# Kernel tuning notes

Hardware: AMD Instinct MI355X
Metric: run time of the kernel (lower is better)

## Reference

```python
import jax, jax.numpy as jnp
import numpy as np

IGNORE_INDEX = -100


def setup_inputs() -> dict:
    key = jax.random.key(0)
    k1, k2, k3 = jax.random.split(key, 3)
    BT, H, V = 2048, 2048, 128000
    x = jax.random.normal(k1, (BT, H), dtype=jnp.float32)
    weight = jax.random.normal(k2, (V, H), dtype=jnp.float32) * (1.0 / np.sqrt(H))
    target = jax.random.randint(k3, (BT,), 0, V, dtype=jnp.int64)
    return {"x": x, "weight": weight, "target": target}


def reference(x, weight, target):
    # Fused linear + cross-entropy forward (reduction='mean').
    # logits: [BT, V], accumulated in fp32 like the helion kernel.
    logits = jnp.einsum("bh,vh->bv", x.astype(jnp.float32), weight.astype(jnp.float32))
    lse = jax.nn.logsumexp(logits, axis=-1)  # [BT]
    target_logit = jnp.take_along_axis(logits, target[:, None], axis=-1)[:, 0]
    valid = (target != IGNORE_INDEX)
    nll = (lse - target_logit) * valid.astype(jnp.float32)  # [BT]
    n_non_ignore = valid.sum().astype(jnp.float32)
    loss = nll.sum() / n_non_ignore
    return loss.astype(x.dtype), lse
```

## Files before the change

### kernel.cpp

```cpp
#include <hip/hip_runtime.h>
#include <hip/hip_bf16.h>


typedef __bf16 bf16x8 __attribute__((ext_vector_type(8)));
typedef float f32x4  __attribute__((ext_vector_type(4)));
typedef float f32x16 __attribute__((ext_vector_type(16)));

#define BM 128
#define BN 128
#define BK 32
#define LDK 40

__device__ __forceinline__ unsigned pkbf(float a, float b) {
  __hip_bfloat162 h = __float22bfloat162_rn(float2{a, b});
  unsigned r;
  __builtin_memcpy(&r, &h, 4);
  return r;
}

__device__ __forceinline__ void gl16(const void* g, const void* l) {
  using GP = const unsigned __attribute__((address_space(1)))*;
  using LP = unsigned __attribute__((address_space(3)))*;
  __builtin_amdgcn_global_load_lds((GP)(unsigned long long)g,
                                   (LP)(unsigned)(unsigned long long)l, 16, 0, 0);
}

__global__ __launch_bounds__(256)
void k_cvt256(const float* __restrict__ src, __bf16* __restrict__ dst, int H, int NT)
{
  const int bid = blockIdx.x;
  const int kt = bid % NT;
  const int r = threadIdx.x;
  const float* s = src + (size_t)((bid / NT) * 256 + r) * H + kt * 64;
  __bf16* d = dst + (size_t)bid * 16384;
  #pragma unroll
  for (int j = 0; j < 8; ++j) {
    float4 f0 = ((const float4*)s)[2 * j];
    float4 f1 = ((const float4*)s)[2 * j + 1];
    uint4 p;
    p.x = pkbf(f0.x, f0.y); p.y = pkbf(f0.z, f0.w);
    p.z = pkbf(f1.x, f1.y); p.w = pkbf(f1.z, f1.w);
    *(uint4*)(d + (j >> 2) * 8192 + (j & 3) * 2048 + r * 8) = p;
  }
}

__global__ __launch_bounds__(256)
void k_tgt(const float* __restrict__ x, const float* __restrict__ w,
           const int* __restrict__ tgt, float* __restrict__ ws_t, int H)
{
  const int row  = blockIdx.x * 4 + (threadIdx.x >> 6);
  const int lane = threadIdx.x & 63;
  const int tv = tgt[row];
  if (tv == -100) { if (lane == 0) ws_t[row] = 0.f; return; }
  const float* xr = x + (size_t)row * H;
  const float* wr = w + (size_t)tv * H;
  float acc = 0.f;
  for (int j = lane * 4; j < H; j += 256) {
    float4 a = *(const float4*)(xr + j);
    float4 b = *(const float4*)(wr + j);
    acc += a.x * b.x + a.y * b.y + a.z * b.z + a.w * b.w;
  }
  #pragma unroll
  for (int m = 1; m < 64; m <<= 1) acc += __shfl_xor(acc, m, 64);
  if (lane == 0) ws_t[row] = acc;
}

#define VM8 asm volatile("s_waitcnt vmcnt(8)" ::: "memory");
#define VM4 asm volatile("s_waitcnt vmcnt(4)" ::: "memory");
#define VM0 asm volatile("s_waitcnt vmcnt(0)" ::: "memory");
#define NOVM
#define MEMFENCE asm volatile("" ::: "memory");

#define SLOT(SL, SLN, BCUR, BNXT, DO_ST, ST_S, DO_RA, VMW)                      \
  {                                                                             \
    __builtin_amdgcn_s_barrier();                                               \
    MEMFENCE                                                                    \
    if (DO_ST) stage_slot(ST_S);                                                \
    _Pragma("unroll")                                                           \
    for (int m = 0; m < 4; ++m)                                                 \
      a1[m] = *(const bf16x8*)&As[SL][kcoff + (arow + (m + 4) * 16) * 8];       \
    __builtin_amdgcn_s_setprio(1);                                              \
    _Pragma("unroll")                                                           \
    for (int m = 0; m < 4; ++m)                                                 \
      _Pragma("unroll")                                                         \
      for (int n = 0; n < 4; ++n)                                               \
        acc[m][n] = __builtin_amdgcn_mfma_f32_16x16x32_bf16(a0[m], BCUR[n],     \
                                                            acc[m][n], 0, 0, 0);\
    __builtin_amdgcn_s_setprio(0);                                              \
    VMW                                                                         \
    __builtin_amdgcn_s_barrier();                                               \
    MEMFENCE                                                                    \
    if (DO_RA) {                                                                \
      _Pragma("unroll")                                                         \
      for (int m = 0; m < 4; ++m)                                               \
        a0[m] = *(const bf16x8*)&As[SLN][kcoff + (arow + m * 16) * 8];          \
      _Pragma("unroll")                                                         \
      for (int n = 0; n < 4; ++n)                                               \
        BNXT[n] = *(const bf16x8*)&Bs[SLN][kcoff + (bcol + n * 16) * 8];        \
    }                                                                           \
    __builtin_amdgcn_s_setprio(1);                                              \
    _Pragma("unroll")                                                           \
    for (int m = 0; m < 4; ++m)                                                 \
      _Pragma("unroll")                                                         \
      for (int n = 0; n < 4; ++n)                                               \
        acc[m + 4][n] = __builtin_amdgcn_mfma_f32_16x16x32_bf16(a1[m], BCUR[n], \
                                                         acc[m + 4][n], 0, 0, 0);\
    __builtin_amdgcn_s_setprio(0);                                              \
  }

__global__ __launch_bounds__(512, 2)
void k_gemm16(const __bf16* __restrict__ xb, const __bf16* __restrict__ wb,
              float* __restrict__ ws_m, float* __restrict__ ws_s,
              int NT, int NCB, int ROWB)
{
  __shared__ __bf16 As[4][8192];
  __shared__ __bf16 Bs[4][8192];

  int wg = blockIdx.x;
  const int nwg = gridDim.x;
  if ((nwg & 7) == 0) wg = (wg & 7) * (nwg >> 3) + (wg >> 3);
  const int rowb = wg % ROWB;
  const int cb   = wg / ROWB;
  const int row0 = rowb * 256;

  const int t    = threadIdx.x;
  const int lane = t & 63;
  const int wv   = t >> 6;
  const int wr   = wv >> 2;
  const int wc   = wv & 3;

  const int kcoff = (lane >> 4) * 2048;
  const int arow  = wr * 128 + (lane & 15);
  const int bcol  = wc * 64 + (lane & 15);

  const __bf16* ga = xb + (size_t)(rowb * NT) * 16384;
  const __bf16* gb = wb + (size_t)(cb * NT) * 16384;

  auto stage_slot = [&](int s) {
    const int ph = s & 3;
    const size_t off = (size_t)(s >> 1) * 16384 + (size_t)(s & 1) * 8192
                     + wv * 512 + lane * 8;
    const __bf16* a = ga + off;
    const __bf16* b = gb + off;
    gl16(a,        &As[ph][wv * 512]);
    gl16(a + 4096, &As[ph][4096 + wv * 512]);
    gl16(b,        &Bs[ph][wv * 512]);
    gl16(b + 4096, &Bs[ph][4096 + wv * 512]);
  };

  const int S = NT * 2;

  stage_slot(0); stage_slot(1); stage_slot(2);
  VM8
  __builtin_amdgcn_s_barrier();
  MEMFENCE

  f32x4 acc[8][4] = {};
  bf16x8 a0[4], a1[4], b0[4], b1[4];
  #pragma unroll
  for (int m = 0; m < 4; ++m)
    a0[m] = *(const bf16x8*)&As[0][kcoff + (arow + m * 16) * 8];
  #pragma unroll
  for (int n = 0; n < 4; ++n)
    b0[n] = *(const bf16x8*)&Bs[0][kcoff + (bcol + n * 16) * 8];

  for (int g = 0; g < (S - 4) / 4; ++g) {
    const int j0 = g * 4;
    SLOT(0, 1, b0, b1, true, j0 + 3, true, VM8)
    SLOT(1, 2, b1, b0, true, j0 + 4, true, VM8)
    SLOT(2, 3, b0, b1, true, j0 + 5, true, VM8)
    SLOT(3, 0, b1, b0, true, j0 + 6, true, VM8)
  }
  SLOT(0, 1, b0, b1, true,  S - 1, true,  VM8)
  SLOT(1, 2, b1, b0, false, 0,     true,  VM4)
  SLOT(2, 3, b0, b1, false, 0,     true,  VM0)
  SLOT(3, 0, b1, b0, false, 0,     false, NOVM)

  __syncthreads();

  float* redM = (float*)&As[0][0];
  float* redS = redM + 1024;
  const int g4 = (lane >> 4) * 4;
  #pragma unroll
  for (int m = 0; m < 8; ++m) {
    #pragma unroll
    for (int r = 0; r < 4; ++r) {
      const int rl = wr * 128 + m * 16 + g4 + r;
      float mx = fmaxf(fmaxf(acc[m][0][r], acc[m][1][r]),
                       fmaxf(acc[m][2][r], acc[m][3][r]));
      #pragma unroll
      for (int sh = 1; sh < 16; sh <<= 1) mx = fmaxf(mx, __shfl_xor(mx, sh, 64));
      float sv = 0.f;
      #pragma unroll
      for (int n = 0; n < 4; ++n) sv += expf(acc[m][n][r] - mx);
      #pragma unroll
      for (int sh = 1; sh < 16; sh <<= 1) sv += __shfl_xor(sv, sh, 64);
      if ((lane & 15) == 0) { redM[wc * 256 + rl] = mx; redS[wc * 256 + rl] = sv; }
    }
  }
  __syncthreads();
  if (t < 256) {
    const float m0 = redM[t], m1 = redM[256 + t], m2 = redM[512 + t], m3 = redM[768 + t];
    float M = fmaxf(fmaxf(m0, m1), fmaxf(m2, m3));
    float S2 = redS[t] * expf(m0 - M) + redS[256 + t] * expf(m1 - M)
             + redS[512 + t] * expf(m2 - M) + redS[768 + t] * expf(m3 - M);
    const int grow = row0 + t;
    ws_m[(size_t)grow * NCB + cb] = M;
    ws_s[(size_t)grow * NCB + cb] = S2;
  }
}

__global__ __launch_bounds__(256, 2)
void k_gemm_lse(const float* __restrict__ x, const float* __restrict__ w,
                const int* __restrict__ tgt,
                float* __restrict__ ws_m, float* __restrict__ ws_s,
                float* __restrict__ ws_t,
                int H, int NCB, int ROWB)
{
  __shared__ unsigned short As[2][BM * LDK];
  __shared__ unsigned short Bs[2][BN * LDK];

  const int bid  = blockIdx.x;
  const int rowb = bid % ROWB;
  const int cb   = bid / ROWB;
  const int row0 = rowb * BM;
  const int col0 = cb * BN;

  const int t    = threadIdx.x;
  const int lane = t & 63;
  const int wv   = t >> 6;
  const int sr = t >> 1;
  const int sk = (t & 1) * 16;

  const float* xa = x + (size_t)(row0 + sr) * H + sk;
  const float* wb = w + (size_t)(col0 + sr) * H + sk;

  float4 ra[4], rb[4];
  #pragma unroll
  for (int i = 0; i < 4; ++i) {
    ra[i] = *(const float4*)(xa + i * 4);
    rb[i] = *(const float4*)(wb + i * 4);
  }

  auto stage = [&](int buf) {
    uint4 p0, p1;
    p0.x = pkbf(ra[0].x, ra[0].y); p0.y = pkbf(ra[0].z, ra[0].w);
    p0.z = pkbf(ra[1].x, ra[1].y); p0.w = pkbf(ra[1].z, ra[1].w);
    p1.x = pkbf(ra[2].x, ra[2].y); p1.y = pkbf(ra[2].z, ra[2].w);
    p1.z = pkbf(ra[3].x, ra[3].y); p1.w = pkbf(ra[3].z, ra[3].w);
    *(uint4*)&As[buf][sr * LDK + sk]     = p0;
    *(uint4*)&As[buf][sr * LDK + sk + 8] = p1;
    p0.x = pkbf(rb[0].x, rb[0].y); p0.y = pkbf(rb[0].z, rb[0].w);
    p0.z = pkbf(rb[1].x, rb[1].y); p0.w = pkbf(rb[1].z, rb[1].w);
    p1.x = pkbf(rb[2].x, rb[2].y); p1.y = pkbf(rb[2].z, rb[2].w);
    p1.z = pkbf(rb[3].x, rb[3].y); p1.w = pkbf(rb[3].z, rb[3].w);
    *(uint4*)&Bs[buf][sr * LDK + sk]     = p0;
    *(uint4*)&Bs[buf][sr * LDK + sk + 8] = p1;
  };

  stage(0);
  __syncthreads();

  f32x16 acc[4] = {};
  const int rlo = lane & 31;
  const int hi  = lane >> 5;
  const int NT  = H / BK;
  int cur = 0;

  for (int kt = 0; kt < NT; ++kt) {
    const bool pf = (kt + 1 < NT);
    if (pf) {
      xa += BK; wb += BK;
      #pragma unroll
      for (int i = 0; i < 4; ++i) {
        ra[i] = *(const float4*)(xa + i * 4);
        rb[i] = *(const float4*)(wb + i * 4);
      }
    }
    const unsigned short* A = As[cur];
    const unsigned short* B = Bs[cur];
    #pragma unroll
    for (int ks = 0; ks < 2; ++ks) {
      const int koff = ks * 16 + hi * 8;
      bf16x8 a = *(const bf16x8*)&A[(wv * 32 + rlo) * LDK + koff];
      #pragma unroll
      for (int nf = 0; nf < 4; ++nf) {
        bf16x8 b = *(const bf16x8*)&B[(nf * 32 + rlo) * LDK + koff];
        acc[nf] = __builtin_amdgcn_mfma_f32_32x32x16_bf16(a, b, acc[nf], 0, 0, 0);
      }
    }
    if (pf) stage(cur ^ 1);
    __syncthreads();
    cur ^= 1;
  }

  #pragma unroll
  for (int reg = 0; reg < 16; ++reg) {
    const int row = wv * 32 + (reg & 3) + 8 * (reg >> 2) + 4 * hi;
    float mx = fmaxf(fmaxf(acc[0][reg], acc[1][reg]), fmaxf(acc[2][reg], acc[3][reg]));
    #pragma unroll
    for (int m = 1; m < 32; m <<= 1) mx = fmaxf(mx, __shfl_xor(mx, m, 64));
    float s = 0.f;
    #pragma unroll
    for (int nf = 0; nf < 4; ++nf) s += expf(acc[nf][reg] - mx);
    #pragma unroll
    for (int m = 1; m < 32; m <<= 1) s += __shfl_xor(s, m, 64);
    const int grow = row0 + row;
    if (rlo == 0) {
      ws_m[(size_t)grow * NCB + cb] = mx;
      ws_s[(size_t)grow * NCB + cb] = s;
    }
    const int tv = tgt[grow];
    #pragma unroll
    for (int nf = 0; nf < 4; ++nf) {
      if (tv == col0 + nf * 32 + rlo) ws_t[grow] = acc[nf][reg];
    }
  }
}

__global__ void k_rowlse(const float* __restrict__ ws_m, const float* __restrict__ ws_s,
                         const float* __restrict__ ws_t, const int* __restrict__ tgt,
                         float* __restrict__ out, float* __restrict__ ws_nll, int NCB)
{
  const int row = blockIdx.x;
  const int t = threadIdx.x;
  const float* pm = ws_m + (size_t)row * NCB;
  const float* ps = ws_s + (size_t)row * NCB;
  __shared__ float red[8];

  float M = -3.0e38f;
  for (int j = t; j < NCB; j += 256) M = fmaxf(M, pm[j]);
  #pragma unroll
  for (int m = 1; m < 64; m <<= 1) M = fmaxf(M, __shfl_xor(M, m, 64));
  if ((t & 63) == 0) red[t >> 6] = M;
  __syncthreads();
  M = fmaxf(fmaxf(red[0], red[1]), fmaxf(red[2], red[3]));

  float S = 0.f;
  for (int j = t; j < NCB; j += 256) S += ps[j] * expf(pm[j] - M);
  #pragma unroll
  for (int m = 1; m < 64; m <<= 1) S += __shfl_xor(S, m, 64);
  if ((t & 63) == 0) red[4 + (t >> 6)] = S;
  __syncthreads();

  if (t == 0) {
    S = red[4] + red[5] + red[6] + red[7];
    const float lse = M + logf(S);
    out[1 + row] = lse;
    const int tv = tgt[row];
    ws_nll[row] = (tv != -100) ? (lse - ws_t[row]) : 0.f;
  }
}

__global__ void k_loss(const float* __restrict__ ws_nll, const int* __restrict__ tgt,
                       float* __restrict__ out, int BT)
{
  const int t = threadIdx.x;
  float s = 0.f, c = 0.f;
  for (int i = t; i < BT; i += 256) {
    s += ws_nll[i];
    c += (tgt[i] != -100) ? 1.f : 0.f;
  }
  __shared__ float rs[4], rc[4];
  #pragma unroll
  for (int m = 1; m < 64; m <<= 1) { s += __shfl_xor(s, m, 64); c += __shfl_xor(c, m, 64); }
  if ((t & 63) == 0) { rs[t >> 6] = s; rc[t >> 6] = c; }
  __syncthreads();
  if (t == 0) {
    s = rs[0] + rs[1] + rs[2] + rs[3];
    c = rc[0] + rc[1] + rc[2] + rc[3];
    out[0] = s / c;
  }
}

extern "C" void kernel_launch(void* const* d_in, const int* in_sizes, int n_in,
                              void* d_out, int out_size, void* d_ws, size_t ws_size,
                              hipStream_t stream)
{
  const float* x  = (const float*)d_in[0];
  const float* w  = (const float*)d_in[1];
  const int* tgt  = (const int*)d_in[2];
  float* out      = (float*)d_out;

  const int BT = in_sizes[2];
  const int H  = in_sizes[0] / BT;
  const int V  = in_sizes[1] / H;

  const int NT    = H / 64;
  const int ROWB  = BT / 256;
  const int NCB   = V / 256;

  const size_t bf_elems   = (size_t)BT * H + (size_t)V * H;
  const size_t need_bytes = bf_elems * 2 + ((size_t)2 * BT * NCB + 2 * (size_t)BT) * 4;

  if (ws_size >= need_bytes && (BT % 256) == 0 && (V % 256) == 0 && (H % 128) == 0) {
    __bf16* x_bf = (__bf16*)d_ws;
    __bf16* w_bf = x_bf + (size_t)BT * H;
    float* ws_m   = (float*)(w_bf + (size_t)V * H);
    float* ws_s   = ws_m + (size_t)BT * NCB;
    float* ws_t   = ws_s + (size_t)BT * NCB;
    float* ws_nll = ws_t + BT;

    k_cvt256<<<(V / 256) * NT, 256, 0, stream>>>(w, w_bf, H, NT);
    k_cvt256<<<(BT / 256) * NT, 256, 0, stream>>>(x, x_bf, H, NT);
    k_tgt<<<BT / 4, 256, 0, stream>>>(x, w, tgt, ws_t, H);
    k_gemm16<<<ROWB * NCB, 512, 0, stream>>>(x_bf, w_bf, ws_m, ws_s, NT, NCB, ROWB);
    k_rowlse<<<BT, 256, 0, stream>>>(ws_m, ws_s, ws_t, tgt, out, ws_nll, NCB);
    k_loss<<<1, 256, 0, stream>>>(ws_nll, tgt, out, BT);
  } else {
    const int ROWB1 = BT / BM;
    const int NCB1  = V / BN;
    float* ws_m   = (float*)d_ws;
    float* ws_s   = ws_m + (size_t)BT * NCB1;
    float* ws_t   = ws_s + (size_t)BT * NCB1;
    float* ws_nll = ws_t + BT;

    k_gemm_lse<<<ROWB1 * NCB1, 256, 0, stream>>>(x, w, tgt, ws_m, ws_s, ws_t, H, NCB1, ROWB1);
    k_rowlse<<<BT, 256, 0, stream>>>(ws_m, ws_s, ws_t, tgt, out, ws_nll, NCB1);
    k_loss<<<1, 256, 0, stream>>>(ws_nll, tgt, out, BT);
  }
}
```

Measured before the change: 1.315 ms.

## Switch GEMM to 32x32x16 MFMA and move staging after compute

Replaces the 16x16x32 bf16 MFMA tiles with 32x32x16 MFMA in the main LSE GEMM, remapping LDS fragment addressing and the epilogue row reduction to the 32-wide output layout. It also moves the global-to-LDS stage issue after the first MFMA batch, drops the leading barrier, and shrinks the prefetch depth from three slots to two with a matching vmcnt wait. The larger MFMA shape is meant to cut LDS reads per FLOP and instruction overhead. The shallower prefetch may expose more memory latency.

```diff
diff --git a/kernel.cpp b/kernel.cpp
--- a/kernel.cpp
+++ b/kernel.cpp
@@ -3,7 +3,6 @@
 
 
 typedef __bf16 bf16x8 __attribute__((ext_vector_type(8)));
-typedef float f32x4  __attribute__((ext_vector_type(4)));
 typedef float f32x16 __attribute__((ext_vector_type(16)));
 
 #define BM 128
@@ -24,6 +23,11 @@
   __builtin_amdgcn_global_load_lds((GP)(unsigned long long)g,
                                    (LP)(unsigned)(unsigned long long)l, 16, 0, 0);
 }
+
+#define VM4 asm volatile("s_waitcnt vmcnt(4)" ::: "memory");
+#define VM0 asm volatile("s_waitcnt vmcnt(0)" ::: "memory");
+#define NOVM
+#define MEMFENCE asm volatile("" ::: "memory");
 
 __global__ __launch_bounds__(256)
 void k_cvt256(const float* __restrict__ src, __bf16* __restrict__ dst, int H, int NT)
@@ -65,53 +69,52 @@
   if (lane == 0) ws_t[row] = acc;
 }
 
-#define VM8 asm volatile("s_waitcnt vmcnt(8)" ::: "memory");
-#define VM4 asm volatile("s_waitcnt vmcnt(4)" ::: "memory");
-#define VM0 asm volatile("s_waitcnt vmcnt(0)" ::: "memory");
-#define NOVM
-#define MEMFENCE asm volatile("" ::: "memory");
-
 #define SLOT(SL, SLN, BCUR, BNXT, DO_ST, ST_S, DO_RA, VMW)                      \
   {                                                                             \
-    __builtin_amdgcn_s_barrier();                                               \
-    MEMFENCE                                                                    \
-    if (DO_ST) stage_slot(ST_S);                                                \
     _Pragma("unroll")                                                           \
-    for (int m = 0; m < 4; ++m)                                                 \
-      a1[m] = *(const bf16x8*)&As[SL][kcoff + (arow + (m + 4) * 16) * 8];       \
+    for (int mk = 0; mk < 4; ++mk)                                              \
+      a1[mk] = *(const bf16x8*)&As[SL][(mk & 1) * 4096 + hi2048 +               \
+                                       (arow + (2 + (mk >> 1)) * 32) * 8];      \
     __builtin_amdgcn_s_setprio(1);                                              \
     _Pragma("unroll")                                                           \
-    for (int m = 0; m < 4; ++m)                                                 \
+    for (int m = 0; m < 2; ++m)                                                 \
       _Pragma("unroll")                                                         \
-      for (int n = 0; n < 4; ++n)                                               \
-        acc[m][n] = __builtin_amdgcn_mfma_f32_16x16x32_bf16(a0[m], BCUR[n],     \
-                                                            acc[m][n], 0, 0, 0);\
+      for (int n = 0; n < 2; ++n)                                               \
+        _Pragma("unroll")                                                       \
+        for (int ks = 0; ks < 2; ++ks)                                          \
+          acc[m][n] = __builtin_amdgcn_mfma_f32_32x32x16_bf16(                  \
+              a0[m * 2 + ks], BCUR[n * 2 + ks], acc[m][n], 0, 0, 0);            \
     __builtin_amdgcn_s_setprio(0);                                              \
+    if (DO_ST) stage_slot(ST_S);                                                \
     VMW                                                                         \
     __builtin_amdgcn_s_barrier();                                               \
     MEMFENCE                                                                    \
     if (DO_RA) {                                                                \
       _Pragma("unroll")                                                         \
-      for (int m = 0; m < 4; ++m)                                               \
-        a0[m] = *(const bf16x8*)&As[SLN][kcoff + (arow + m * 16) * 8];          \
+      for (int mk = 0; mk < 4; ++mk)                                            \
+        a0[mk] = *(const bf16x8*)&As[SLN][(mk & 1) * 4096 + hi2048 +            \
+                                          (arow + (mk >> 1) * 32) * 8];         \
       _Pragma("unroll")                                                         \
-      for (int n = 0; n < 4; ++n)                                               \
-        BNXT[n] = *(const bf16x8*)&Bs[SLN][kcoff + (bcol + n * 16) * 8];        \
+      for (int nk = 0; nk < 4; ++nk)                                            \
+        BNXT[nk] = *(const bf16x8*)&Bs[SLN][(nk & 1) * 4096 + hi2048 +          \
+                                            (bcol + (nk >> 1) * 32) * 8];       \
     }                                                                           \
     __builtin_amdgcn_s_setprio(1);                                              \
     _Pragma("unroll")                                                           \
-    for (int m = 0; m < 4; ++m)                                                 \
+    for (int m = 0; m < 2; ++m)                                                 \
       _Pragma("unroll")                                                         \
-      for (int n = 0; n < 4; ++n)                                               \
-        acc[m + 4][n] = __builtin_amdgcn_mfma_f32_16x16x32_bf16(a1[m], BCUR[n], \
-                                                         acc[m + 4][n], 0, 0, 0);\
+      for (int n = 0; n < 2; ++n)                                               \
+        _Pragma("unroll")                                                       \
+        for (int ks = 0; ks < 2; ++ks)                                          \
+          acc[m + 2][n] = __builtin_amdgcn_mfma_f32_32x32x16_bf16(              \
+              a1[m * 2 + ks], BCUR[n * 2 + ks], acc[m + 2][n], 0, 0, 0);        \
     __builtin_amdgcn_s_setprio(0);                                              \
   }
 
 __global__ __launch_bounds__(512, 2)
-void k_gemm16(const __bf16* __restrict__ xb, const __bf16* __restrict__ wb,
+void k_gemm32(const __bf16* __restrict__ xb, const __bf16* __restrict__ wb,
               float* __restrict__ ws_m, float* __restrict__ ws_s,
-              int NT, int NCB, int ROWB)
+              int S, int NCB, int ROWB)
 {
   __shared__ __bf16 As[4][8192];
   __shared__ __bf16 Bs[4][8192];
@@ -128,13 +131,14 @@
   const int wv   = t >> 6;
   const int wr   = wv >> 2;
   const int wc   = wv & 3;
-
-  const int kcoff = (lane >> 4) * 2048;
-  const int arow  = wr * 128 + (lane & 15);
-  const int bcol  = wc * 64 + (lane & 15);
-
-  const __bf16* ga = xb + (size_t)(rowb * NT) * 16384;
-  const __bf16* gb = wb + (size_t)(cb * NT) * 16384;
+  const int rlo  = lane & 31;
+  const int hi   = lane >> 5;
+  const int hi2048 = hi * 2048;
+  const int arow = wr * 128 + rlo;
+  const int bcol = wc * 64 + rlo;
+
+  const __bf16* ga = xb + (size_t)(rowb * (S / 2)) * 16384;
+  const __bf16* gb = wb + (size_t)(cb * (S / 2)) * 16384;
 
   auto stage_slot = [&](int s) {
     const int ph = s & 3;
@@ -148,31 +152,31 @@
     gl16(b + 4096, &Bs[ph][4096 + wv * 512]);
   };
 
-  const int S = NT * 2;
-
-  stage_slot(0); stage_slot(1); stage_slot(2);
-  VM8
+  stage_slot(0); stage_slot(1);
+  VM4
   __builtin_amdgcn_s_barrier();
   MEMFENCE
 
-  f32x4 acc[8][4] = {};
+  f32x16 acc[4][2] = {};
   bf16x8 a0[4], a1[4], b0[4], b1[4];
   #pragma unroll
-  for (int m = 0; m < 4; ++m)
-    a0[m] = *(const bf16x8*)&As[0][kcoff + (arow + m * 16) * 8];
-  #pragma unroll
-  for (int n = 0; n < 4; ++n)
-    b0[n] = *(const bf16x8*)&Bs[0][kcoff + (bcol + n * 16) * 8];
+  for (int mk = 0; mk < 4; ++mk)
+    a0[mk] = *(const bf16x8*)&As[0][(mk & 1) * 4096 + hi2048 +
+                                    (arow + (mk >> 1) * 32) * 8];
+  #pragma unroll
+  for (int nk = 0; nk < 4; ++nk)
+    b0[nk] = *(const bf16x8*)&Bs[0][(nk & 1) * 4096 + hi2048 +
+                                    (bcol + (nk >> 1) * 32) * 8];
 
   for (int g = 0; g < (S - 4) / 4; ++g) {
     const int j0 = g * 4;
-    SLOT(0, 1, b0, b1, true, j0 + 3, true, VM8)
-    SLOT(1, 2, b1, b0, true, j0 + 4, true, VM8)
-    SLOT(2, 3, b0, b1, true, j0 + 5, true, VM8)
-    SLOT(3, 0, b1, b0, true, j0 + 6, true, VM8)
-  }
-  SLOT(0, 1, b0, b1, true,  S - 1, true,  VM8)
-  SLOT(1, 2, b1, b0, false, 0,     true,  VM4)
+    SLOT(0, 1, b0, b1, true, j0 + 2, true, VM4)
+    SLOT(1, 2, b1, b0, true, j0 + 3, true, VM4)
+    SLOT(2, 3, b0, b1, true, j0 + 4, true, VM4)
+    SLOT(3, 0, b1, b0, true, j0 + 5, true, VM4)
+  }
+  SLOT(0, 1, b0, b1, true,  S - 2, true,  VM4)
+  SLOT(1, 2, b1, b0, true,  S - 1, true,  VM4)
   SLOT(2, 3, b0, b1, false, 0,     true,  VM0)
   SLOT(3, 0, b1, b0, false, 0,     false, NOVM)
 
@@ -180,22 +184,19 @@
 
   float* redM = (float*)&As[0][0];
   float* redS = redM + 1024;
-  const int g4 = (lane >> 4) * 4;
-  #pragma unroll
-  for (int m = 0; m < 8; ++m) {
-    #pragma unroll
-    for (int r = 0; r < 4; ++r) {
-      const int rl = wr * 128 + m * 16 + g4 + r;
-      float mx = fmaxf(fmaxf(acc[m][0][r], acc[m][1][r]),
-                       fmaxf(acc[m][2][r], acc[m][3][r]));
+  #pragma unroll
+  for (int mr = 0; mr < 4; ++mr) {
+    #pragma unroll
+    for (int reg = 0; reg < 16; ++reg) {
+      const int rl = wr * 128 + mr * 32 + (reg & 3) + 8 * (reg >> 2) + 4 * hi;
+      const float v0 = acc[mr][0][reg], v1 = acc[mr][1][reg];
+      float mx = fmaxf(v0, v1);
       #pragma unroll
-      for (int sh = 1; sh < 16; sh <<= 1) mx = fmaxf(mx, __shfl_xor(mx, sh, 64));
-      float sv = 0.f;
+      for (int m = 1; m < 32; m <<= 1) mx = fmaxf(mx, __shfl_xor(mx, m, 64));
+      float sv = expf(v0 - mx) + expf(v1 - mx);
       #pragma unroll
-      for (int n = 0; n < 4; ++n) sv += expf(acc[m][n][r] - mx);
-      #pragma unroll
-      for (int sh = 1; sh < 16; sh <<= 1) sv += __shfl_xor(sv, sh, 64);
-      if ((lane & 15) == 0) { redM[wc * 256 + rl] = mx; redS[wc * 256 + rl] = sv; }
+      for (int m = 1; m < 32; m <<= 1) sv += __shfl_xor(sv, m, 64);
+      if (rlo == 0) { redM[wc * 256 + rl] = mx; redS[wc * 256 + rl] = sv; }
     }
   }
   __syncthreads();
@@ -404,7 +405,8 @@
     k_cvt256<<<(V / 256) * NT, 256, 0, stream>>>(w, w_bf, H, NT);
     k_cvt256<<<(BT / 256) * NT, 256, 0, stream>>>(x, x_bf, H, NT);
     k_tgt<<<BT / 4, 256, 0, stream>>>(x, w, tgt, ws_t, H);
-    k_gemm16<<<ROWB * NCB, 512, 0, stream>>>(x_bf, w_bf, ws_m, ws_s, NT, NCB, ROWB);
+    k_gemm32<<<ROWB * NCB, 512, 0, stream>>>(x_bf, w_bf, ws_m, ws_s,
+                                             NT * 2, NCB, ROWB);
     k_rowlse<<<BT, 256, 0, stream>>>(ws_m, ws_s, ws_t, tgt, out, ws_nll, NCB);
     k_loss<<<1, 256, 0, stream>>>(ws_nll, tgt, out, BT);
   } else {
```

After: 1.553 ms. 1.18x slower.
